# Kernel tuning notes

Measured on AMD Instinct MI355X. Metric: run time of the kernel, lower is better.

The kernel has to match this reference:

```python
import jax, jax.numpy as jnp
import numpy as np

B, S, W = 64, 20, 1024   # batch, max_seq, num_words
NC = 80                  # num_cls
DL, DE = 300, 128        # dim_latent, dim_embed


def setup_inputs() -> dict:
    key = jax.random.key(0)
    ks = jax.random.split(key, 12)
    inp = {
        "word_recon": jax.random.normal(ks[0], (B, S, W), jnp.float32),
        "beta_pri": jnp.float32(0.3),
        "metrix_sl": jax.random.uniform(ks[1], (NC, W), jnp.float32),
        "cls_word_prob": jax.random.uniform(ks[2], (NC, W), jnp.float32),
        # learned params (nn.init.normal_(w, 0, 0.01); biases zero-ish)
        "emb_table": 0.01 * jax.random.normal(ks[3], (W + 1, DL), jnp.float32),
        "w_sl": 0.01 * jax.random.normal(ks[4], (NC, W), jnp.float32),
        "b_sl": jnp.zeros((NC,), jnp.float32),
        "w_lw": 0.01 * jax.random.normal(ks[5], (DE, DL), jnp.float32),
        "b_lw": jnp.zeros((DE,), jnp.float32),
        "w_gcn": 0.01 * jax.random.normal(ks[6], (DE, DE * W), jnp.float32),
        "b_gcn": jnp.zeros((DE,), jnp.float32),
        "w_cls": 0.01 * jax.random.normal(ks[7], (NC, DE), jnp.float32),
        "b_cls": jnp.zeros((NC,), jnp.float32),
        "label": jax.random.randint(ks[8], (B,), 0, NC),
        "k": 20,
    }
    return inp


def reference(word_recon, beta_pri, metrix_sl, cls_word_prob, emb_table,
              w_sl, b_sl, w_lw, b_lw, w_gcn, b_gcn, w_cls, b_cls, label, k):
    b = word_recon.shape[0]
    # compute_adj: argmax word id per timestep, keep first k positions
    ids = jnp.argmax(word_recon, axis=2)[:, :k]                     # [B,k] int
    multi_hot = jnp.zeros((b, W), jnp.int32).at[
        jnp.arange(b)[:, None], ids].set(1)                          # [B,W]
    mh_f = multi_hot.astype(word_recon.dtype)
    # adj = eye + all-pairs among selected words (idempotent set-to-1)
    adj = jnp.maximum(jnp.eye(W, dtype=mh_f.dtype),
                      mh_f[:, :, None] * mh_f[:, None, :])           # [B,W,W]
    # vectorized replacement of the per-sample mm loop
    weight_cls = jax.nn.softmax(mh_f @ w_sl.T + b_sl, axis=1)        # [B,NC]
    weight_pri = weight_cls @ metrix_sl                              # [B,W]
    adj_pri = weight_pri[:, :, None] * weight_pri[:, None, :]        # [B,W,W]
    word_prob = cls_word_prob[label]                                 # [B,W]
    adj_mix = (1.0 - beta_pri) * adj + beta_pri * adj_pri
    # GCN layer: embedding gather (indices are 0/1, faithful to source)
    embed = emb_table[multi_hot]                                     # [B,W,DL]
    support = embed @ w_lw.T + b_lw                                  # [B,W,DE]
    feat = jax.nn.leaky_relu(jnp.einsum('bij,bjd->bid', adj_mix, support))
    # dropout disabled (eval mode)
    feat = jax.nn.leaky_relu(feat.reshape(b, -1) @ w_gcn.T + b_gcn)  # [B,DE]
    output = feat @ w_cls.T + b_cls                                  # [B,NC]
    return (output, feat, weight_pri[:, None, :], adj_pri, word_prob[:, None, :])
```

## Files before the change

### kernel.cpp

```cpp
#include <hip/hip_runtime.h>
#include <cstdint>

#define BB   64
#define SS   20
#define WW   1024
#define NCC  80
#define DLL  300
#define DEE  128
#define KMAX 20

#define O_OUT   0
#define O_FEAT  (BB*NCC)
#define O_WP    (O_FEAT + BB*DEE)
#define O_ADJ   (O_WP + BB*WW)
#define O_WPROB ((size_t)O_ADJ + (size_t)BB*WW*WW)

#define WS_V    0
#define WS_S0   (WS_V + BB*DEE)
#define WS_S1   (WS_S0 + DEE)
#define WS_N1   (WS_S1 + DEE)
#define WS_MHT  (WS_N1 + 64)
#define WS_WPT  (WS_MHT + WW*BB)
#define WS_P    (WS_WPT + WW*BB)
#define MM_BLOCKS 512

__device__ __forceinline__ void amax2(float& v, int& i, float ov, int oi) {
    if (ov > v || (ov == v && oi < i)) { v = ov; i = oi; }
}

__device__ __forceinline__ float lrelu(float x) {
    return x >= 0.f ? x : 0.01f * x;
}

__global__ __launch_bounds__(256) void k1_prep(
    const float* __restrict__ word_recon, const float* __restrict__ metrix_sl,
    const float* __restrict__ cls_word_prob, const float* __restrict__ emb,
    const float* __restrict__ w_sl, const float* __restrict__ b_sl,
    const float* __restrict__ w_lw, const float* __restrict__ b_lw,
    const int* __restrict__ label, const int* __restrict__ kptr,
    float* __restrict__ out, float* __restrict__ ws)
{
    const int b = blockIdx.x, t = threadIdx.x;
    __shared__ __align__(16) float l_mh[WW];
    __shared__ __align__(16) float l_wp[WW];
    __shared__ float l_wc[NCC];
    __shared__ __align__(16) float l_s0[DEE];
    __shared__ __align__(16) float l_s1[DEE];
    __shared__ int   l_ids[KMAX];
    __shared__ int   l_cnt;
    __shared__ float l_av[4];
    __shared__ int   l_ai[4];
    __shared__ float l_red[4];
    __shared__ float l_max, l_sum, l_sw1, l_swall;

    for (int w = t; w < WW; w += 256) l_mh[w] = 0.f;
    if (t == 0) l_cnt = 0;
    __syncthreads();

    int kk = kptr[0];
    if (kk > SS) kk = SS;
    if (kk > KMAX) kk = KMAX;

    for (int s = 0; s < kk; ++s) {
        const float* row = word_recon + ((size_t)b * SS + s) * WW;
        float4 x = *(const float4*)(row + t * 4);
        float bv = x.x; int bi = t * 4;
        amax2(bv, bi, x.y, t * 4 + 1);
        amax2(bv, bi, x.z, t * 4 + 2);
        amax2(bv, bi, x.w, t * 4 + 3);
        for (int off = 32; off >= 1; off >>= 1) {
            float ov = __shfl_down(bv, off);
            int   oi = __shfl_down(bi, off);
            amax2(bv, bi, ov, oi);
        }
        if ((t & 63) == 0) { l_av[t >> 6] = bv; l_ai[t >> 6] = bi; }
        __syncthreads();
        if (t == 0) {
            float v0 = l_av[0]; int i0 = l_ai[0];
            amax2(v0, i0, l_av[1], l_ai[1]);
            amax2(v0, i0, l_av[2], l_ai[2]);
            amax2(v0, i0, l_av[3], l_ai[3]);
            if (l_mh[i0] == 0.f) { l_mh[i0] = 1.f; l_ids[l_cnt++] = i0; }
        }
        __syncthreads();
    }
    const int n1 = l_cnt;

    {
        float* mh_T = ws + WS_MHT;
        for (int w = t; w < WW; w += 256) mh_T[w * BB + b] = l_mh[w];
        if (t == 0) (ws + WS_N1)[b] = (float)n1;
    }

    if (t < NCC) {
        float lg = b_sl[t];
        for (int u = 0; u < n1; ++u) lg += w_sl[t * WW + l_ids[u]];
        l_wc[t] = lg;
    }
    __syncthreads();
    if (t == 0) {
        float m = l_wc[0];
        for (int c = 1; c < NCC; ++c) m = fmaxf(m, l_wc[c]);
        l_max = m;
    }
    __syncthreads();
    if (t < NCC) l_wc[t] = expf(l_wc[t] - l_max);
    __syncthreads();
    if (t == 0) {
        float s = 0.f;
        for (int c = 0; c < NCC; ++c) s += l_wc[c];
        l_sum = s;
    }
    __syncthreads();
    if (t < NCC) l_wc[t] = l_wc[t] / l_sum;
    __syncthreads();

    float swpart;
    {
        int w4 = t * 4;
        float4 acc = {0.f, 0.f, 0.f, 0.f};
        for (int c = 0; c < NCC; ++c) {
            float wc = l_wc[c];
            float4 m4 = *(const float4*)(metrix_sl + c * WW + w4);
            acc.x += wc * m4.x; acc.y += wc * m4.y;
            acc.z += wc * m4.z; acc.w += wc * m4.w;
        }
        *(float4*)(out + O_WP + b * WW + w4) = acc;
        *(float4*)(&l_wp[w4]) = acc;
        float* wp_T = ws + WS_WPT;
        wp_T[(w4 + 0) * BB + b] = acc.x;
        wp_T[(w4 + 1) * BB + b] = acc.y;
        wp_T[(w4 + 2) * BB + b] = acc.z;
        wp_T[(w4 + 3) * BB + b] = acc.w;
        swpart = acc.x + acc.y + acc.z + acc.w;
    }
    for (int off = 32; off >= 1; off >>= 1) swpart += __shfl_down(swpart, off);
    if ((t & 63) == 0) l_red[t >> 6] = swpart;
    __syncthreads();
    if (t == 0) {
        float sa = l_red[0] + l_red[1] + l_red[2] + l_red[3];
        float s1v = 0.f;
        for (int u = 0; u < n1; ++u) s1v += l_wp[l_ids[u]];
        l_swall = sa; l_sw1 = s1v;
    }
    __syncthreads();

    if (t < DEE) {
        float a0 = b_lw[t], a1 = b_lw[t];
        const float* wl = w_lw + t * DLL;
        for (int l = 0; l < DLL; l += 4) {
            float4 wv = *(const float4*)(wl + l);
            float4 e0 = *(const float4*)(emb + l);
            float4 e1 = *(const float4*)(emb + DLL + l);
            a0 += wv.x * e0.x + wv.y * e0.y + wv.z * e0.z + wv.w * e0.w;
            a1 += wv.x * e1.x + wv.y * e1.y + wv.z * e1.z + wv.w * e1.w;
        }
        l_s0[t] = a0; l_s1[t] = a1;
        if (b == 0) { (ws + WS_S0)[t] = a0; (ws + WS_S1)[t] = a1; }
    }
    __syncthreads();

    if (t < DEE) {
        float sw1 = l_sw1, sw0 = l_swall - l_sw1;
        (ws + WS_V)[b * DEE + t] = l_s1[t] * sw1 + l_s0[t] * sw0;
    }

    {
        int lbl = label[b];
        int w4 = t * 4;
        float4 p4 = *(const float4*)(cls_word_prob + (size_t)lbl * WW + w4);
        *(float4*)(out + O_WPROB + (size_t)b * WW + w4) = p4;
    }
}

__global__ __launch_bounds__(256) void k_adj(
    const float* __restrict__ wp, float* __restrict__ adj)
{
    const int t = threadIdx.x;
    const int base_row = blockIdx.x * 8;
#pragma unroll
    for (int n = 0; n < 8; ++n) {
        int r = base_row + n;
        int b = r >> 10, i = r & 1023;
        float wi = wp[b * WW + i];
        float4 v4 = *(const float4*)(wp + b * WW + t * 4);
        float4 o;
        o.x = wi * v4.x; o.y = wi * v4.y; o.z = wi * v4.z; o.w = wi * v4.w;
        *(float4*)(adj + ((size_t)r << 10) + t * 4) = o;
    }
}

__global__ __launch_bounds__(256) void k_mm(
    const float* __restrict__ w_gcn, const float* __restrict__ beta_p,
    const float* __restrict__ vv, const float* __restrict__ s0g,
    const float* __restrict__ s1g, const float* __restrict__ n1g,
    const float* __restrict__ mh_T, const float* __restrict__ wp_T,
    float* __restrict__ P)
{
    __shared__ __align__(16) float F[DEE * BB];
    __shared__ __align__(16) float s0s[DEE];
    __shared__ __align__(16) float s1s[DEE];
    const int t = threadIdx.x;
    if (t < DEE) { s0s[t] = s0g[t]; s1s[t] = s1g[t]; }
    const float beta = beta_p[0];
    const float omb = 1.f - beta;

    float c[4][8];
#pragma unroll
    for (int a = 0; a < 4; ++a)
#pragma unroll
        for (int q = 0; q < 8; ++q) c[a][q] = 0.f;

    const int b0 = (t & 15) * 4;
    const int d0 = (t >> 4) * 8;
    const int fb = t >> 2;
    const int e0 = (t & 3) * 32;
    __syncthreads();

    for (int ii = 0; ii < 2; ++ii) {
        const int i = blockIdx.x * 2 + ii;
        {
            float p    = mh_T[i * BB + fb];
            float wpbi = wp_T[i * BB + fb];
            float n1   = n1g[fb];
            float a1 = omb * p * n1;
            float a0 = omb * (1.f - p);
            float g  = beta * wpbi;
#pragma unroll
            for (int q = 0; q < 32; q += 4) {
                int e = e0 + q;
                float4 v4  = *(const float4*)(vv + fb * DEE + e);
                float4 s04 = *(const float4*)(&s0s[e]);
                float4 s14 = *(const float4*)(&s1s[e]);
                F[(e + 0) * BB + fb] = lrelu(a1 * s14.x + a0 * s04.x + g * v4.x);
                F[(e + 1) * BB + fb] = lrelu(a1 * s14.y + a0 * s04.y + g * v4.y);
                F[(e + 2) * BB + fb] = lrelu(a1 * s14.z + a0 * s04.z + g * v4.z);
                F[(e + 3) * BB + fb] = lrelu(a1 * s14.w + a0 * s04.w + g * v4.w);
            }
        }
        __syncthreads();
        const float* gbase = w_gcn + (size_t)i * DEE;
#pragma unroll 2
        for (int e4 = 0; e4 < 32; ++e4) {
            int e = e4 * 4;
            float4 f0 = *(const float4*)(&F[(e + 0) * BB + b0]);
            float4 f1 = *(const float4*)(&F[(e + 1) * BB + b0]);
            float4 f2 = *(const float4*)(&F[(e + 2) * BB + b0]);
            float4 f3 = *(const float4*)(&F[(e + 3) * BB + b0]);
#pragma unroll
            for (int q = 0; q < 8; ++q) {
                float4 g4 = *(const float4*)(gbase + (size_t)(d0 + q) * (DEE * WW) + e);
                c[0][q] += f0.x * g4.x + f1.x * g4.y + f2.x * g4.z + f3.x * g4.w;
                c[1][q] += f0.y * g4.x + f1.y * g4.y + f2.y * g4.z + f3.y * g4.w;
                c[2][q] += f0.z * g4.x + f1.z * g4.y + f2.z * g4.z + f3.z * g4.w;
                c[3][q] += f0.w * g4.x + f1.w * g4.y + f2.w * g4.z + f3.w * g4.w;
            }
        }
        __syncthreads();
    }

    float* pb = P + (size_t)blockIdx.x * (BB * DEE);
#pragma unroll
    for (int jb = 0; jb < 4; ++jb) {
        float4 lo = {c[jb][0], c[jb][1], c[jb][2], c[jb][3]};
        float4 hi = {c[jb][4], c[jb][5], c[jb][6], c[jb][7]};
        *(float4*)(pb + (b0 + jb) * DEE + d0)     = lo;
        *(float4*)(pb + (b0 + jb) * DEE + d0 + 4) = hi;
    }
}

__global__ __launch_bounds__(1024) void k_red(
    const float* __restrict__ P, const float* __restrict__ b_gcn,
    const float* __restrict__ w_cls, const float* __restrict__ b_cls,
    float* __restrict__ out)
{
    const int b = blockIdx.x, t = threadIdx.x;
    const int d = t & 127, pg = t >> 7;
    __shared__ float red[8][DEE];
    __shared__ __align__(16) float lf[DEE];

    const float* pp = P + (size_t)pg * 64 * (BB * DEE) + b * DEE + d;
    float a0 = 0.f, a1 = 0.f, a2 = 0.f, a3 = 0.f;
    for (int p = 0; p < 64; p += 4) {
        a0 += pp[(size_t)(p + 0) * (BB * DEE)];
        a1 += pp[(size_t)(p + 1) * (BB * DEE)];
        a2 += pp[(size_t)(p + 2) * (BB * DEE)];
        a3 += pp[(size_t)(p + 3) * (BB * DEE)];
    }
    red[pg][d] = (a0 + a1) + (a2 + a3);
    __syncthreads();
    if (t < DEE) {
        float s = 0.f;
#pragma unroll
        for (int g = 0; g < 8; ++g) s += red[g][t];
        s += b_gcn[t];
        s = lrelu(s);
        out[O_FEAT + b * DEE + t] = s;
        lf[t] = s;
    }
    __syncthreads();
    if (t < NCC) {
        float o = b_cls[t];
        const float* wc = w_cls + t * DEE;
        for (int d2 = 0; d2 < DEE; d2 += 4) {
            float4 w4 = *(const float4*)(wc + d2);
            o += w4.x * lf[d2] + w4.y * lf[d2 + 1] + w4.z * lf[d2 + 2] + w4.w * lf[d2 + 3];
        }
        out[b * NCC + t] = o;
    }
}

extern "C" void kernel_launch(void* const* d_in, const int* in_sizes, int n_in,
                              void* d_out, int out_size, void* d_ws, size_t ws_size,
                              hipStream_t stream) {
    const float* word_recon    = (const float*)d_in[0];
    const float* beta_p        = (const float*)d_in[1];
    const float* metrix_sl     = (const float*)d_in[2];
    const float* cls_word_prob = (const float*)d_in[3];
    const float* emb           = (const float*)d_in[4];
    const float* w_sl          = (const float*)d_in[5];
    const float* b_sl          = (const float*)d_in[6];
    const float* w_lw          = (const float*)d_in[7];
    const float* b_lw          = (const float*)d_in[8];
    const float* w_gcn         = (const float*)d_in[9];
    const float* b_gcn         = (const float*)d_in[10];
    const float* w_cls         = (const float*)d_in[11];
    const float* b_cls         = (const float*)d_in[12];
    const int*   label         = (const int*)d_in[13];
    const int*   kptr          = (const int*)d_in[14];
    float* out = (float*)d_out;
    float* ws  = (float*)d_ws;

    k1_prep<<<BB, 256, 0, stream>>>(word_recon, metrix_sl, cls_word_prob, emb,
                                    w_sl, b_sl, w_lw, b_lw, label, kptr, out, ws);
    k_adj<<<(BB * WW) / 8, 256, 0, stream>>>(out + O_WP, out + O_ADJ);
    k_mm<<<MM_BLOCKS, 256, 0, stream>>>(w_gcn, beta_p, ws + WS_V, ws + WS_S0,
                                        ws + WS_S1, ws + WS_N1, ws + WS_MHT,
                                        ws + WS_WPT, ws + WS_P);
    k_red<<<BB, 1024, 0, stream>>>(ws + WS_P, b_gcn, w_cls, b_cls, out);
}
```

Measured before the change: 455.5 us.

## Fuse adj_pri outer-product writes into GEMM kernel with nontemporal stores

Removes the separate k_adj kernel and folds its writes into the w_gcn GEMM kernel. Each of the 512 blocks writes 128 rows of adj_pri, interleaved with the inner GEMM loop, so the 256MB store stream overlaps the w_gcn read stream. The stores are nontemporal to avoid polluting the cache. Both phases are bandwidth bound, so the benefit depends on overlap rather than on total traffic, and the interleaving may cut GEMM issue efficiency.

```diff
diff --git a/kernel.cpp b/kernel.cpp
--- a/kernel.cpp
+++ b/kernel.cpp
@@ -23,6 +23,8 @@
 #define WS_WPT  (WS_MHT + WW*BB)
 #define WS_P    (WS_WPT + WW*BB)
 #define MM_BLOCKS 512
+
+typedef float nfloat4 __attribute__((ext_vector_type(4)));
 
 __device__ __forceinline__ void amax2(float& v, int& i, float ov, int oi) {
     if (ov > v || (ov == v && oi < i)) { v = ov; i = oi; }
@@ -173,37 +175,27 @@
     }
 }
 
-__global__ __launch_bounds__(256) void k_adj(
-    const float* __restrict__ wp, float* __restrict__ adj)
-{
-    const int t = threadIdx.x;
-    const int base_row = blockIdx.x * 8;
-#pragma unroll
-    for (int n = 0; n < 8; ++n) {
-        int r = base_row + n;
-        int b = r >> 10, i = r & 1023;
-        float wi = wp[b * WW + i];
-        float4 v4 = *(const float4*)(wp + b * WW + t * 4);
-        float4 o;
-        o.x = wi * v4.x; o.y = wi * v4.y; o.z = wi * v4.z; o.w = wi * v4.w;
-        *(float4*)(adj + ((size_t)r << 10) + t * 4) = o;
-    }
-}
-
-__global__ __launch_bounds__(256) void k_mm(
+__global__ __launch_bounds__(256) void k_fused(
     const float* __restrict__ w_gcn, const float* __restrict__ beta_p,
     const float* __restrict__ vv, const float* __restrict__ s0g,
     const float* __restrict__ s1g, const float* __restrict__ n1g,
     const float* __restrict__ mh_T, const float* __restrict__ wp_T,
+    const float* __restrict__ wp, float* __restrict__ adj,
     float* __restrict__ P)
 {
     __shared__ __align__(16) float F[DEE * BB];
     __shared__ __align__(16) float s0s[DEE];
     __shared__ __align__(16) float s1s[DEE];
+    __shared__ __align__(16) float wi_s[128];
     const int t = threadIdx.x;
     if (t < DEE) { s0s[t] = s0g[t]; s1s[t] = s1g[t]; }
     const float beta = beta_p[0];
     const float omb = 1.f - beta;
+
+    const int b_adj  = blockIdx.x >> 3;
+    const int i0_adj = (blockIdx.x & 7) * 128;
+    if (t < 128) wi_s[t] = wp[b_adj * WW + i0_adj + t];
+    const float4 wrow = *(const float4*)(wp + b_adj * WW + t * 4);
 
     float c[4][8];
 #pragma unroll
@@ -239,9 +231,23 @@
             }
         }
         __syncthreads();
+
         const float* gbase = w_gcn + (size_t)i * DEE;
+        const size_t rbase = ((size_t)(b_adj << 10) + i0_adj + ii * 64);
 #pragma unroll 2
         for (int e4 = 0; e4 < 32; ++e4) {
+            {
+                const int n0 = e4 * 2;
+#pragma unroll
+                for (int n = 0; n < 2; ++n) {
+                    const float wi = wi_s[ii * 64 + n0 + n];
+                    nfloat4 o;
+                    o.x = wi * wrow.x; o.y = wi * wrow.y;
+                    o.z = wi * wrow.z; o.w = wi * wrow.w;
+                    __builtin_nontemporal_store(
+                        o, (nfloat4*)(adj + ((rbase + n0 + n) << 10) + t * 4));
+                }
+            }
             int e = e4 * 4;
             float4 f0 = *(const float4*)(&F[(e + 0) * BB + b0]);
             float4 f1 = *(const float4*)(&F[(e + 1) * BB + b0]);
@@ -333,9 +339,9 @@
 
     k1_prep<<<BB, 256, 0, stream>>>(word_recon, metrix_sl, cls_word_prob, emb,
                                     w_sl, b_sl, w_lw, b_lw, label, kptr, out, ws);
-    k_adj<<<(BB * WW) / 8, 256, 0, stream>>>(out + O_WP, out + O_ADJ);
-    k_mm<<<MM_BLOCKS, 256, 0, stream>>>(w_gcn, beta_p, ws + WS_V, ws + WS_S0,
-                                        ws + WS_S1, ws + WS_N1, ws + WS_MHT,
-                                        ws + WS_WPT, ws + WS_P);
+    k_fused<<<MM_BLOCKS, 256, 0, stream>>>(w_gcn, beta_p, ws + WS_V, ws + WS_S0,
+                                           ws + WS_S1, ws + WS_N1, ws + WS_MHT,
+                                           ws + WS_WPT, out + O_WP, out + O_ADJ,
+                                           ws + WS_P);
     k_red<<<BB, 1024, 0, stream>>>(ws + WS_P, b_gcn, w_cls, b_cls, out);
 }
```

Result: no change. 449.9 us (-1.2%).
